# Optimization experiments

Measured on AMD Instinct MI355X. Metric: run time of the kernel, lower is better.

## Reference

```python
import jax, jax.numpy as jnp
import numpy as np

N, E, R, D = 100000, 300000, 2, 128


def setup_inputs() -> dict:
    key = jax.random.key(0)
    k0, k1, k2, k3, k4 = jax.random.split(key, 5)
    x = jax.random.normal(k0, (N, D), dtype=jnp.float32)
    attn_w = jax.random.normal(k1, (R, 2 * D), dtype=jnp.float32) / np.sqrt(2 * D).astype(np.float32)
    loop_weight = jax.random.normal(k2, (D, D), dtype=jnp.float32) / np.sqrt(D).astype(np.float32)
    h_bias = jnp.zeros((D,), dtype=jnp.float32)
    src = jax.random.randint(k3, (R, E), 0, N, dtype=jnp.int32)
    dst = jax.random.randint(k4, (R, E), 0, N, dtype=jnp.int32)
    return {"x": x, "attn_w": attn_w, "loop_weight": loop_weight, "h_bias": h_bias,
            "src": src, "dst": dst}


def _rel_attention(x, a, src_r, dst_r):
    # Per-edge score: attn_fc(cat(src feat, dst feat)) with Linear(2D -> 1, no bias).
    d = x.shape[1]
    xs = x[src_r]                     # [E, D] gathered source features (the messages m)
    e = xs @ a[:d] + x[dst_r] @ a[d:]  # [E] edge logits (note: no leaky_relu in message_fc path)
    # Segment (per-destination mailbox) softmax, numerically stable.
    m = jax.ops.segment_max(e, dst_r, num_segments=N)
    p = jnp.exp(e - m[dst_r])
    denom = jax.ops.segment_sum(p, dst_r, num_segments=N)
    alpha = p / jnp.maximum(denom[dst_r], jnp.float32(1e-30))  # [E]
    # Weighted scatter-sum of messages back to destination nodes.
    return jax.ops.segment_sum(alpha[:, None] * xs, dst_r, num_segments=N)  # [N, D]


def reference(x, attn_w, loop_weight, h_bias, src, dst):
    # multi_update_all(..., 'sum'): sum the per-relation attention aggregations.
    agg = _rel_attention(x, attn_w[0], src[0], dst[0])
    for r in range(1, R):
        agg = agg + _rel_attention(x, attn_w[r], src[r], dst[r])
    # self loop + bias (activation=None, dropout=0)
    h = agg + x @ loop_weight + h_bias
    return h
```

## Files before the change

kernel.cpp:

```cpp
#include <hip/hip_runtime.h>

#define N_NODES 100000
#define N_EDGES 300000
#define DIM     128
#define NBINS   (2 * N_NODES)
#define CNT_STRIDE 8
#define SLOT_CAP 24
#define ROW_TILES (N_NODES / 16)
#define GDIM (DIM + 4)

#define WCONV_BLOCKS 8
#define BIN_BLOCKS  ((N_EDGES + 255) / 256)
#define SCORE_BLOCKS (N_NODES / 4)

typedef __attribute__((ext_vector_type(8))) short bfrag;
typedef __attribute__((ext_vector_type(4))) float f32x4;
typedef __attribute__((ext_vector_type(2))) float f32x2;
typedef __attribute__((ext_vector_type(2))) unsigned int   u32x2;

__device__ __forceinline__ unsigned short f2bf(float f) {
  unsigned int u = __float_as_uint(f);
  u += 0x7FFFu + ((u >> 16) & 1u);
  return (unsigned short)(u >> 16);
}
__device__ __forceinline__ float bflo(unsigned int u) { return __uint_as_float(u << 16); }
__device__ __forceinline__ float bfhi(unsigned int u) { return __uint_as_float(u & 0xffff0000u); }

__global__ __launch_bounds__(256) void k1_kernel(
    const float* __restrict__ x, const float* __restrict__ attn_w,
    const float* __restrict__ W,
    const int* __restrict__ src, const int* __restrict__ dst,
    float* __restrict__ pexp, int* __restrict__ counts, int* __restrict__ slots,
    unsigned short* __restrict__ Wt, unsigned short* __restrict__ x_bf) {
  if (blockIdx.x < WCONV_BLOCKS) {
    for (int e = blockIdx.x * 256 + threadIdx.x; e < DIM * DIM; e += WCONV_BLOCKS * 256) {
      int k = e >> 7, c = e & 127;
      Wt[c * DIM + k] = f2bf(W[e]);
    }
    return;
  }
  if (blockIdx.x < WCONV_BLOCKS + BIN_BLOCKS) {
    int e = (blockIdx.x - WCONV_BLOCKS) * 256 + threadIdx.x;
    if (e < N_EDGES) {
      int d0 = __builtin_nontemporal_load(&dst[e]);
      int d1 = __builtin_nontemporal_load(&dst[e + N_EDGES]);
      int s0 = __builtin_nontemporal_load(&src[e]);
      int s1 = __builtin_nontemporal_load(&src[e + N_EDGES]);
      int p0 = atomicAdd(&counts[(size_t)(d0 * 2 + 0) * CNT_STRIDE], 1);
      int p1 = atomicAdd(&counts[(size_t)(d1 * 2 + 1) * CNT_STRIDE], 1);
      if (p0 < SLOT_CAP)
        __builtin_nontemporal_store(s0, &slots[(size_t)(d0 * 2 + 0) * SLOT_CAP + p0]);
      if (p1 < SLOT_CAP)
        __builtin_nontemporal_store(s1, &slots[(size_t)(d1 * 2 + 1) * SLOT_CAP + p1]);
    }
    return;
  }
  int wave = (((blockIdx.x - WCONV_BLOCKS - BIN_BLOCKS) * 256) + (int)threadIdx.x) >> 6;
  int lane = threadIdx.x & 63;
  if (wave >= N_NODES) return;
  f32x2 a0 = ((const f32x2*)(attn_w +   0))[lane];
  f32x2 a1 = ((const f32x2*)(attn_w + 256))[lane];
  f32x2 v = __builtin_nontemporal_load(((const f32x2*)(x + (size_t)wave * DIM)) + lane);
  ushort2 bv; bv.x = f2bf(v.x); bv.y = f2bf(v.y);
  ((ushort2*)(x_bf + (size_t)wave * DIM))[lane] = bv;
  float p0 = v.x * a0.x + v.y * a0.y;
  float p1 = v.x * a1.x + v.y * a1.y;
  #pragma unroll
  for (int off = 32; off > 0; off >>= 1) {
    p0 += __shfl_down(p0, off, 64);
    p1 += __shfl_down(p1, off, 64);
  }
  if (lane == 0) {
    pexp[wave]           = __expf(p0);
    pexp[N_NODES + wave] = __expf(p1);
  }
}

__global__ __launch_bounds__(256) void k2_kernel(
    const int* __restrict__ slots, const int* __restrict__ counts,
    const float* __restrict__ pexp, const unsigned short* __restrict__ x_bf,
    const unsigned short* __restrict__ Wt, const float* __restrict__ bias,
    float* __restrict__ out) {
  __shared__ float gtile[16][GDIM];
  int tid = threadIdx.x;
  int r0  = blockIdx.x * 16;
  int w   = tid >> 6;
  int wl  = tid & 63;
  {
    int n = wl & 15, q = wl >> 4;
    const unsigned short* xrow = x_bf + (size_t)(r0 + n) * DIM;
    f32x4 acc[2];
    #pragma unroll
    for (int c = 0; c < 2; c++) {
      float bv = bias[(2 * w + c) * 16 + n];
      acc[c] = (f32x4){bv, bv, bv, bv};
    }
    #pragma unroll
    for (int kc = 0; kc < 4; kc++) {
      int k0 = kc * 32 + q * 8;
      bfrag a = *((const bfrag*)(xrow + k0));
      #pragma unroll
      for (int c = 0; c < 2; c++) {
        bfrag b = *((const bfrag*)(Wt + (size_t)((2 * w + c) * 16 + n) * DIM + k0));
        acc[c] = __builtin_amdgcn_mfma_f32_16x16x32_bf16(a, b, acc[c], 0, 0, 0);
      }
    }
    #pragma unroll
    for (int c = 0; c < 2; c++)
      #pragma unroll
      for (int rr = 0; rr < 4; rr++)
        gtile[q * 4 + rr][(2 * w + c) * 16 + n] = acc[c][rr];
  }
  __syncthreads();
  int rrel  = wl >> 5;
  int l     = wl & 31;
  int nbase = r0 + w * 4;
  int craw[4], sraw[4];
  #pragma unroll
  for (int nn = 0; nn < 4; nn++)
    craw[nn] = counts[(size_t)((nbase + nn) * 2 + rrel) * CNT_STRIDE];
  #pragma unroll
  for (int nn = 0; nn < 4; nn++)
    sraw[nn] = slots[(size_t)((nbase + nn) * 2 + rrel) * SLOT_CAP + l];
  int cnt[4]; int sj[4];
  #pragma unroll
  for (int nn = 0; nn < 4; nn++) {
    cnt[nn] = (craw[nn] > SLOT_CAP) ? SLOT_CAP : craw[nn];
    sj[nn]  = (l < cnt[nn]) ? sraw[nn] : 0;
  }
  float pl[4];
  #pragma unroll
  for (int nn = 0; nn < 4; nn++)
    pl[nn] = pexp[rrel * N_NODES + sj[nn]];
  float pj[4]; float dinv[4];
  #pragma unroll
  for (int nn = 0; nn < 4; nn++) {
    pj[nn] = (l < cnt[nn]) ? pl[nn] : 0.f;
    float d = pj[nn];
    #pragma unroll
    for (int off = 16; off > 0; off >>= 1) d += __shfl_xor(d, off, 64);
    dinv[nn] = (cnt[nn] > 0) ? 1.f / d : 0.f;
  }
  u32x2 g[4][4];
  #pragma unroll
  for (int u = 0; u < 4; u++) {
    #pragma unroll
    for (int nn = 0; nn < 4; nn++) {
      int s = __shfl(sj[nn], u, 32);
      g[nn][u] = ((const u32x2*)(x_bf + (size_t)s * DIM))[l];
    }
  }
  f32x4 accr[4];
  #pragma unroll
  for (int nn = 0; nn < 4; nn++) accr[nn] = (f32x4){0.f, 0.f, 0.f, 0.f};
  #pragma unroll
  for (int nn = 0; nn < 4; nn++) {
    #pragma unroll
    for (int u = 0; u < 4; u++) {
      float qv = __shfl(pj[nn], u, 32);
      u32x2 gv = g[nn][u];
      accr[nn].x += qv * bflo(gv.x);
      accr[nn].y += qv * bfhi(gv.x);
      accr[nn].z += qv * bflo(gv.y);
      accr[nn].w += qv * bfhi(gv.y);
    }
  }
  #pragma unroll
  for (int nn = 0; nn < 4; nn++) {
    int cn = cnt[nn];
    int j = 4;
    for (; j + 4 <= cn; j += 4) {
      int   s0 = __shfl(sj[nn], j + 0, 32); float q0 = __shfl(pj[nn], j + 0, 32);
      int   s1 = __shfl(sj[nn], j + 1, 32); float q1 = __shfl(pj[nn], j + 1, 32);
      int   s2 = __shfl(sj[nn], j + 2, 32); float q2 = __shfl(pj[nn], j + 2, 32);
      int   s3 = __shfl(sj[nn], j + 3, 32); float q3 = __shfl(pj[nn], j + 3, 32);
      u32x2 g0 = ((const u32x2*)(x_bf + (size_t)s0 * DIM))[l];
      u32x2 g1 = ((const u32x2*)(x_bf + (size_t)s1 * DIM))[l];
      u32x2 g2 = ((const u32x2*)(x_bf + (size_t)s2 * DIM))[l];
      u32x2 g3 = ((const u32x2*)(x_bf + (size_t)s3 * DIM))[l];
      accr[nn].x += q0*bflo(g0.x) + q1*bflo(g1.x) + q2*bflo(g2.x) + q3*bflo(g3.x);
      accr[nn].y += q0*bfhi(g0.x) + q1*bfhi(g1.x) + q2*bfhi(g2.x) + q3*bfhi(g3.x);
      accr[nn].z += q0*bflo(g0.y) + q1*bflo(g1.y) + q2*bflo(g2.y) + q3*bflo(g3.y);
      accr[nn].w += q0*bfhi(g0.y) + q1*bfhi(g1.y) + q2*bfhi(g2.y) + q3*bfhi(g3.y);
    }
    for (; j < cn; j++) {
      int   s0 = __shfl(sj[nn], j, 32); float q0 = __shfl(pj[nn], j, 32);
      u32x2 g0 = ((const u32x2*)(x_bf + (size_t)s0 * DIM))[l];
      accr[nn].x += q0*bflo(g0.x); accr[nn].y += q0*bfhi(g0.x);
      accr[nn].z += q0*bflo(g0.y); accr[nn].w += q0*bfhi(g0.y);
    }
  }
  #pragma unroll
  for (int nn = 0; nn < 4; nn++) {
    f32x4 agg;
    agg.x = accr[nn].x * dinv[nn];
    agg.y = accr[nn].y * dinv[nn];
    agg.z = accr[nn].z * dinv[nn];
    agg.w = accr[nn].w * dinv[nn];
    agg.x += __shfl_xor(agg.x, 32, 64);
    agg.y += __shfl_xor(agg.y, 32, 64);
    agg.z += __shfl_xor(agg.z, 32, 64);
    agg.w += __shfl_xor(agg.w, 32, 64);
    if (wl < 32) {
      const float* gr = &gtile[w * 4 + nn][4 * wl];
      f32x4 o;
      o.x = gr[0] + agg.x; o.y = gr[1] + agg.y;
      o.z = gr[2] + agg.z; o.w = gr[3] + agg.w;
      __builtin_nontemporal_store(o, (f32x4*)(out + (size_t)(r0 + w * 4 + nn) * DIM) + wl);
    }
  }
}

extern "C" void kernel_launch(void* const* d_in, const int* in_sizes, int n_in,
                              void* d_out, int out_size, void* d_ws, size_t ws_size,
                              hipStream_t stream) {
  const float* x      = (const float*)d_in[0];
  const float* attn_w = (const float*)d_in[1];
  const float* loop_w = (const float*)d_in[2];
  const float* h_bias = (const float*)d_in[3];
  const int*   src    = (const int*)d_in[4];
  const int*   dst    = (const int*)d_in[5];
  float*       out    = (float*)d_out;

  float*          pexp   = (float*)d_ws;
  int*            counts = (int*)(pexp + NBINS);
  int*            slots  = counts + (size_t)NBINS * CNT_STRIDE;
  unsigned short* Wt     = (unsigned short*)(slots + (size_t)NBINS * SLOT_CAP);
  unsigned short* x_bf   = Wt + DIM * DIM;

  hipMemsetAsync(counts, 0, (size_t)NBINS * CNT_STRIDE * sizeof(int), stream);
  k1_kernel<<<WCONV_BLOCKS + BIN_BLOCKS + SCORE_BLOCKS, 256, 0, stream>>>(
      x, attn_w, loop_w, src, dst, pexp, counts, slots, Wt, x_bf);
  k2_kernel<<<ROW_TILES, 256, 0, stream>>>(
      slots, counts, pexp, x_bf, Wt, h_bias, out);
}
```

Baseline: 221.7 us.

## Batch edge binning, grid-stride node scoring, and deepen upfront neighbor gathers

The binning path now has each thread handle two edges per relation, which halves the block count and puts more atomics in flight per thread. Node scoring becomes a persistent grid-stride loop with half-waves per node and 16-byte loads, replacing one wave per node. In the aggregation kernel, the first 8 neighbor rows (up from 4) are gathered up front under a count guard, the 4-way unrolled remainder loop becomes a scalar loop, and counts/slots are read with nontemporal loads. The intent is more memory-level parallelism for the latency-bound gathers and fewer launched blocks, at the cost of more registers and possible occupancy loss.

```diff
diff --git a/kernel.cpp b/kernel.cpp
--- a/kernel.cpp
+++ b/kernel.cpp
@@ -8,14 +8,15 @@
 #define SLOT_CAP 24
 #define ROW_TILES (N_NODES / 16)
 #define GDIM (DIM + 4)
+#define BATCH 8
 
 #define WCONV_BLOCKS 8
-#define BIN_BLOCKS  ((N_EDGES + 255) / 256)
-#define SCORE_BLOCKS (N_NODES / 4)
+#define BIN2_BLOCKS ((N_EDGES / 2 + 255) / 256)
+#define SC_BLOCKS   1024
+#define SC_WAVES    (SC_BLOCKS * 4)
 
 typedef __attribute__((ext_vector_type(8))) short bfrag;
 typedef __attribute__((ext_vector_type(4))) float f32x4;
-typedef __attribute__((ext_vector_type(2))) float f32x2;
 typedef __attribute__((ext_vector_type(2))) unsigned int   u32x2;
 
 __device__ __forceinline__ unsigned short f2bf(float f) {
@@ -32,47 +33,65 @@
     const int* __restrict__ src, const int* __restrict__ dst,
     float* __restrict__ pexp, int* __restrict__ counts, int* __restrict__ slots,
     unsigned short* __restrict__ Wt, unsigned short* __restrict__ x_bf) {
+  int tid = threadIdx.x;
   if (blockIdx.x < WCONV_BLOCKS) {
-    for (int e = blockIdx.x * 256 + threadIdx.x; e < DIM * DIM; e += WCONV_BLOCKS * 256) {
+    for (int e = blockIdx.x * 256 + tid; e < DIM * DIM; e += WCONV_BLOCKS * 256) {
       int k = e >> 7, c = e & 127;
       Wt[c * DIM + k] = f2bf(W[e]);
     }
     return;
   }
-  if (blockIdx.x < WCONV_BLOCKS + BIN_BLOCKS) {
-    int e = (blockIdx.x - WCONV_BLOCKS) * 256 + threadIdx.x;
-    if (e < N_EDGES) {
-      int d0 = __builtin_nontemporal_load(&dst[e]);
-      int d1 = __builtin_nontemporal_load(&dst[e + N_EDGES]);
-      int s0 = __builtin_nontemporal_load(&src[e]);
-      int s1 = __builtin_nontemporal_load(&src[e + N_EDGES]);
-      int p0 = atomicAdd(&counts[(size_t)(d0 * 2 + 0) * CNT_STRIDE], 1);
-      int p1 = atomicAdd(&counts[(size_t)(d1 * 2 + 1) * CNT_STRIDE], 1);
-      if (p0 < SLOT_CAP)
-        __builtin_nontemporal_store(s0, &slots[(size_t)(d0 * 2 + 0) * SLOT_CAP + p0]);
-      if (p1 < SLOT_CAP)
-        __builtin_nontemporal_store(s1, &slots[(size_t)(d1 * 2 + 1) * SLOT_CAP + p1]);
+  if (blockIdx.x < WCONV_BLOCKS + BIN2_BLOCKS) {
+    int t = (blockIdx.x - WCONV_BLOCKS) * 256 + tid;
+    if (t < N_EDGES / 2) {
+      int ea = t, eb = t + N_EDGES / 2;
+      int da0 = __builtin_nontemporal_load(&dst[ea]);
+      int db0 = __builtin_nontemporal_load(&dst[eb]);
+      int da1 = __builtin_nontemporal_load(&dst[ea + N_EDGES]);
+      int db1 = __builtin_nontemporal_load(&dst[eb + N_EDGES]);
+      int sa0 = __builtin_nontemporal_load(&src[ea]);
+      int sb0 = __builtin_nontemporal_load(&src[eb]);
+      int sa1 = __builtin_nontemporal_load(&src[ea + N_EDGES]);
+      int sb1 = __builtin_nontemporal_load(&src[eb + N_EDGES]);
+      int pa0 = atomicAdd(&counts[(size_t)(da0 * 2 + 0) * CNT_STRIDE], 1);
+      int pb0 = atomicAdd(&counts[(size_t)(db0 * 2 + 0) * CNT_STRIDE], 1);
+      int pa1 = atomicAdd(&counts[(size_t)(da1 * 2 + 1) * CNT_STRIDE], 1);
+      int pb1 = atomicAdd(&counts[(size_t)(db1 * 2 + 1) * CNT_STRIDE], 1);
+      if (pa0 < SLOT_CAP)
+        __builtin_nontemporal_store(sa0, &slots[(size_t)(da0 * 2 + 0) * SLOT_CAP + pa0]);
+      if (pb0 < SLOT_CAP)
+        __builtin_nontemporal_store(sb0, &slots[(size_t)(db0 * 2 + 0) * SLOT_CAP + pb0]);
+      if (pa1 < SLOT_CAP)
+        __builtin_nontemporal_store(sa1, &slots[(size_t)(da1 * 2 + 1) * SLOT_CAP + pa1]);
+      if (pb1 < SLOT_CAP)
+        __builtin_nontemporal_store(sb1, &slots[(size_t)(db1 * 2 + 1) * SLOT_CAP + pb1]);
     }
     return;
   }
-  int wave = (((blockIdx.x - WCONV_BLOCKS - BIN_BLOCKS) * 256) + (int)threadIdx.x) >> 6;
-  int lane = threadIdx.x & 63;
-  if (wave >= N_NODES) return;
-  f32x2 a0 = ((const f32x2*)(attn_w +   0))[lane];
-  f32x2 a1 = ((const f32x2*)(attn_w + 256))[lane];
-  f32x2 v = __builtin_nontemporal_load(((const f32x2*)(x + (size_t)wave * DIM)) + lane);
-  ushort2 bv; bv.x = f2bf(v.x); bv.y = f2bf(v.y);
-  ((ushort2*)(x_bf + (size_t)wave * DIM))[lane] = bv;
-  float p0 = v.x * a0.x + v.y * a0.y;
-  float p1 = v.x * a1.x + v.y * a1.y;
-  #pragma unroll
-  for (int off = 32; off > 0; off >>= 1) {
-    p0 += __shfl_down(p0, off, 64);
-    p1 += __shfl_down(p1, off, 64);
-  }
-  if (lane == 0) {
-    pexp[wave]           = __expf(p0);
-    pexp[N_NODES + wave] = __expf(p1);
+  int wave = (((blockIdx.x - WCONV_BLOCKS - BIN2_BLOCKS) * 256) + tid) >> 6;
+  int l    = tid & 63;
+  int h    = l >> 5;
+  int l32  = l & 31;
+  f32x4 a0 = ((const f32x4*)(attn_w +   0))[l32];
+  f32x4 a1 = ((const f32x4*)(attn_w + 256))[l32];
+  for (int base = wave * 2; base < N_NODES; base += SC_WAVES * 2) {
+    int n = base + h;
+    if (n >= N_NODES) continue;
+    f32x4 v = __builtin_nontemporal_load(((const f32x4*)(x + (size_t)n * DIM)) + l32);
+    unsigned int lo = ((unsigned int)f2bf(v.y) << 16) | f2bf(v.x);
+    unsigned int hi = ((unsigned int)f2bf(v.w) << 16) | f2bf(v.z);
+    ((u32x2*)(x_bf + (size_t)n * DIM))[l32] = (u32x2){lo, hi};
+    float p0 = v.x*a0.x + v.y*a0.y + v.z*a0.z + v.w*a0.w;
+    float p1 = v.x*a1.x + v.y*a1.y + v.z*a1.z + v.w*a1.w;
+    #pragma unroll
+    for (int off = 16; off > 0; off >>= 1) {
+      p0 += __shfl_xor(p0, off, 64);
+      p1 += __shfl_xor(p1, off, 64);
+    }
+    if (l32 == 0) {
+      pexp[n]           = __expf(p0);
+      pexp[N_NODES + n] = __expf(p1);
+    }
   }
 }
 
@@ -118,10 +137,12 @@
   int craw[4], sraw[4];
   #pragma unroll
   for (int nn = 0; nn < 4; nn++)
-    craw[nn] = counts[(size_t)((nbase + nn) * 2 + rrel) * CNT_STRIDE];
+    craw[nn] = __builtin_nontemporal_load(
+        &counts[(size_t)((nbase + nn) * 2 + rrel) * CNT_STRIDE]);
   #pragma unroll
   for (int nn = 0; nn < 4; nn++)
-    sraw[nn] = slots[(size_t)((nbase + nn) * 2 + rrel) * SLOT_CAP + l];
+    sraw[nn] = __builtin_nontemporal_load(
+        &slots[(size_t)((nbase + nn) * 2 + rrel) * SLOT_CAP + l]);
   int cnt[4]; int sj[4];
   #pragma unroll
   for (int nn = 0; nn < 4; nn++) {
@@ -141,13 +162,16 @@
     for (int off = 16; off > 0; off >>= 1) d += __shfl_xor(d, off, 64);
     dinv[nn] = (cnt[nn] > 0) ? 1.f / d : 0.f;
   }
-  u32x2 g[4][4];
-  #pragma unroll
-  for (int u = 0; u < 4; u++) {
+  u32x2 g[4][BATCH];
+  #pragma unroll
+  for (int u = 0; u < BATCH; u++) {
     #pragma unroll
     for (int nn = 0; nn < 4; nn++) {
       int s = __shfl(sj[nn], u, 32);
-      g[nn][u] = ((const u32x2*)(x_bf + (size_t)s * DIM))[l];
+      u32x2 gv = (u32x2){0u, 0u};
+      if (u < cnt[nn])
+        gv = ((const u32x2*)(x_bf + (size_t)s * DIM))[l];
+      g[nn][u] = gv;
     }
   }
   f32x4 accr[4];
@@ -156,7 +180,7 @@
   #pragma unroll
   for (int nn = 0; nn < 4; nn++) {
     #pragma unroll
-    for (int u = 0; u < 4; u++) {
+    for (int u = 0; u < BATCH; u++) {
       float qv = __shfl(pj[nn], u, 32);
       u32x2 gv = g[nn][u];
       accr[nn].x += qv * bflo(gv.x);
@@ -168,22 +192,7 @@
   #pragma unroll
   for (int nn = 0; nn < 4; nn++) {
     int cn = cnt[nn];
-    int j = 4;
-    for (; j + 4 <= cn; j += 4) {
-      int   s0 = __shfl(sj[nn], j + 0, 32); float q0 = __shfl(pj[nn], j + 0, 32);
-      int   s1 = __shfl(sj[nn], j + 1, 32); float q1 = __shfl(pj[nn], j + 1, 32);
-      int   s2 = __shfl(sj[nn], j + 2, 32); float q2 = __shfl(pj[nn], j + 2, 32);
-      int   s3 = __shfl(sj[nn], j + 3, 32); float q3 = __shfl(pj[nn], j + 3, 32);
-      u32x2 g0 = ((const u32x2*)(x_bf + (size_t)s0 * DIM))[l];
-      u32x2 g1 = ((const u32x2*)(x_bf + (size_t)s1 * DIM))[l];
-      u32x2 g2 = ((const u32x2*)(x_bf + (size_t)s2 * DIM))[l];
-      u32x2 g3 = ((const u32x2*)(x_bf + (size_t)s3 * DIM))[l];
-      accr[nn].x += q0*bflo(g0.x) + q1*bflo(g1.x) + q2*bflo(g2.x) + q3*bflo(g3.x);
-      accr[nn].y += q0*bfhi(g0.x) + q1*bfhi(g1.x) + q2*bfhi(g2.x) + q3*bfhi(g3.x);
-      accr[nn].z += q0*bflo(g0.y) + q1*bflo(g1.y) + q2*bflo(g2.y) + q3*bflo(g3.y);
-      accr[nn].w += q0*bfhi(g0.y) + q1*bfhi(g1.y) + q2*bfhi(g2.y) + q3*bfhi(g3.y);
-    }
-    for (; j < cn; j++) {
+    for (int j = BATCH; j < cn; j++) {
       int   s0 = __shfl(sj[nn], j, 32); float q0 = __shfl(pj[nn], j, 32);
       u32x2 g0 = ((const u32x2*)(x_bf + (size_t)s0 * DIM))[l];
       accr[nn].x += q0*bflo(g0.x); accr[nn].y += q0*bfhi(g0.x);
@@ -229,7 +238,7 @@
   unsigned short* x_bf   = Wt + DIM * DIM;
 
   hipMemsetAsync(counts, 0, (size_t)NBINS * CNT_STRIDE * sizeof(int), stream);
-  k1_kernel<<<WCONV_BLOCKS + BIN_BLOCKS + SCORE_BLOCKS, 256, 0, stream>>>(
+  k1_kernel<<<WCONV_BLOCKS + BIN2_BLOCKS + SC_BLOCKS, 256, 0, stream>>>(
       x, attn_w, loop_w, src, dst, pexp, counts, slots, Wt, x_bf);
   k2_kernel<<<ROW_TILES, 256, 0, stream>>>(
       slots, counts, pexp, x_bf, Wt, h_bias, out);
```

Result: no change. 225.4 us (+1.7%).
